# Optimization experiments

Measured on AMD Instinct MI355X. Metric: run time of the kernel, lower is better.

## Reference

```python
import jax, jax.numpy as jnp
import numpy as np

D_MODEL = 2048
D_FFN = 8192
RANK = 16
MOD_SCALE = 0.1
EPS = 1e-6


def setup_inputs() -> dict:
    key = jax.random.key(0)
    ks = jax.random.split(key, 8)
    B, S = 2, 2048
    init_scale = 0.01
    return {
        'hidden_states': jax.random.normal(ks[0], (B, S, D_MODEL), jnp.float32),
        'attn_output': jax.random.normal(ks[1], (B, S, D_MODEL), jnp.float32),
        'A': jax.random.normal(ks[2], (D_MODEL, RANK), jnp.float32) * (init_scale / np.sqrt(D_MODEL)),
        'Bmat': jax.random.normal(ks[3], (RANK, D_FFN), jnp.float32) * (init_scale / np.sqrt(RANK)),
        'W_in': jax.random.normal(ks[4], (D_FFN, D_MODEL), jnp.float32) * 0.02,  # gate_proj.weight
        'W_up': jax.random.normal(ks[5], (D_FFN, D_MODEL), jnp.float32) * 0.02,  # up_proj.weight
        'W_down': jax.random.normal(ks[6], (D_MODEL, D_FFN), jnp.float32) * 0.02,  # down_proj.weight
        'gamma': jnp.ones((D_MODEL,), jnp.float32),  # post_attention_layernorm (RMSNorm) weight
    }


def _rmsnorm(x, gamma):
    var = jnp.mean(x * x, axis=-1, keepdims=True)
    return x * jax.lax.rsqrt(var + EPS) * gamma


def reference(hidden_states, attn_output, A, Bmat, W_in, W_up, W_down, gamma):
    residual = hidden_states
    # Neuro-plastic modulation: [B,S,r]
    modulation = MOD_SCALE * jnp.tanh(jnp.einsum('bsd,dr->bsr', attn_output, A))
    # NPT applies post-attn norm to the residual (not residual+attn)
    h = _rmsnorm(residual, gamma)  # [B,S,d_model]
    # Fused per-token weight delta: delta_w^T @ h == B^T ((A^T h) * mod)
    hA = jnp.einsum('bsd,dr->bsr', h, A)  # [B,S,r]
    delta_out = jnp.einsum('bsr,rf->bsf', hA * modulation, Bmat)  # [B,S,d_ffn]
    gate = jax.nn.silu(jnp.einsum('bsd,fd->bsf', h, W_in) + delta_out)
    up = jnp.einsum('bsd,fd->bsf', h, W_up)
    out = jnp.einsum('bsf,df->bsd', gate * up, W_down)
    return residual + out
```

## Files before the change

kernel.cpp:

```cpp
#include <hip/hip_runtime.h>
#include <cstdint>
#include <cstddef>

#define D_MODEL 2048
#define D_FFN   8192
#define RANK    16
#define EPS     1e-6f
#define MOD_SCALE 0.1f

typedef float    f32x4 __attribute__((ext_vector_type(4)));
typedef _Float16 half8 __attribute__((ext_vector_type(8)));

__device__ __forceinline__ void async_load16(const void* g, void* l) {
  __builtin_amdgcn_global_load_lds(
      (const __attribute__((address_space(1))) uint32_t*)g,
      (__attribute__((address_space(3))) uint32_t*)l,
      16, 0, 0);
}

__device__ __forceinline__ void stage_tile(const _Float16* __restrict__ gbase,
                                           size_t stride, _Float16* lds, int tid) {
  #pragma unroll
  for (int j = 0; j < 4; ++j) {
    int idx = j * 256 + tid;
    int row = idx >> 3;
    int c   = (idx & 7) ^ (row & 7);
    async_load16(gbase + (size_t)row * stride + c * 8, &lds[idx * 8]);
  }
}

__device__ __forceinline__ half8 frag_read(const _Float16* lds, int r, int c) {
  return *(const half8*)&lds[r * 64 + ((c ^ (r & 7)) * 8)];
}

__global__ __launch_bounds__(256) void convert3_f32_f16(
    const float* __restrict__ s0, const float* __restrict__ s1,
    const float* __restrict__ s2,
    _Float16* __restrict__ d0, _Float16* __restrict__ d1,
    _Float16* __restrict__ d2)
{
  const int w = blockIdx.x >> 13;
  const float*   s = (w == 0) ? s0 : (w == 1) ? s1 : s2;
  _Float16*      d = (w == 0) ? d0 : (w == 1) ? d1 : d2;
  size_t i = ((size_t)(blockIdx.x & 8191) * 256 + threadIdx.x) * 8;
  f32x4 a = *(const f32x4*)(s + i);
  f32x4 b = *(const f32x4*)(s + i + 4);
  half8 h;
  #pragma unroll
  for (int j = 0; j < 4; ++j) { h[j] = (_Float16)a[j]; h[4+j] = (_Float16)b[j]; }
  *(half8*)(d + i) = h;
}

__global__ __launch_bounds__(256) void convert_f32_f16(
    const float* __restrict__ s, _Float16* __restrict__ d)
{
  size_t i = ((size_t)blockIdx.x * 256 + threadIdx.x) * 8;
  f32x4 a = *(const f32x4*)(s + i);
  f32x4 b = *(const f32x4*)(s + i + 4);
  half8 h;
  #pragma unroll
  for (int j = 0; j < 4; ++j) { h[j] = (_Float16)a[j]; h[4+j] = (_Float16)b[j]; }
  *(half8*)(d + i) = h;
}

__global__ __launch_bounds__(256) void prep_kernel(
    const float* __restrict__ hs, const float* __restrict__ attn,
    const float* __restrict__ Amat, const float* __restrict__ gamma,
    _Float16* __restrict__ h16, float* __restrict__ cmat)
{
  const int token = blockIdx.x;
  const int tid   = threadIdx.x;
  const int lane  = tid & 63;
  const int wv    = tid >> 6;
  const size_t tb = (size_t)token * D_MODEL;
  const int base  = tid * 8;

  f32x4 x0 = *(const f32x4*)(hs + tb + base);
  f32x4 x1 = *(const f32x4*)(hs + tb + base + 4);
  f32x4 a0 = *(const f32x4*)(attn + tb + base);
  f32x4 a1 = *(const f32x4*)(attn + tb + base + 4);

  float ss = 0.f;
  #pragma unroll
  for (int j = 0; j < 4; ++j) ss += x0[j]*x0[j] + x1[j]*x1[j];
  #pragma unroll
  for (int off = 32; off > 0; off >>= 1) ss += __shfl_xor(ss, off, 64);

  __shared__ float red[4];
  __shared__ float redp[4][RANK];
  __shared__ float redh[4][RANK];
  if (lane == 0) red[wv] = ss;
  __syncthreads();
  const float tot = red[0] + red[1] + red[2] + red[3];
  const float rms = rsqrtf(tot * (1.0f / D_MODEL) + EPS);

  f32x4 g0 = *(const f32x4*)(gamma + base);
  f32x4 g1 = *(const f32x4*)(gamma + base + 4);
  float hv[8], av[8];
  #pragma unroll
  for (int j = 0; j < 4; ++j) {
    hv[j]   = x0[j] * rms * g0[j];
    hv[4+j] = x1[j] * rms * g1[j];
    av[j]   = a0[j];
    av[4+j] = a1[j];
  }
  half8 hh;
  #pragma unroll
  for (int j = 0; j < 8; ++j) hh[j] = (_Float16)hv[j];
  *(half8*)(h16 + tb + base) = hh;

  float pa[RANK], ph[RANK];
  #pragma unroll
  for (int r = 0; r < RANK; ++r) { pa[r] = 0.f; ph[r] = 0.f; }
  #pragma unroll
  for (int e = 0; e < 8; ++e) {
    const f32x4* Ar = (const f32x4*)(Amat + (size_t)(base + e) * RANK);
    #pragma unroll
    for (int q = 0; q < 4; ++q) {
      f32x4 ar = Ar[q];
      #pragma unroll
      for (int j = 0; j < 4; ++j) {
        pa[q*4+j] += av[e] * ar[j];
        ph[q*4+j] += hv[e] * ar[j];
      }
    }
  }
  #pragma unroll
  for (int r = 0; r < RANK; ++r) {
    #pragma unroll
    for (int off = 32; off > 0; off >>= 1) {
      pa[r] += __shfl_xor(pa[r], off, 64);
      ph[r] += __shfl_xor(ph[r], off, 64);
    }
  }
  if (lane == 0) {
    #pragma unroll
    for (int r = 0; r < RANK; ++r) { redp[wv][r] = pa[r]; redh[wv][r] = ph[r]; }
  }
  __syncthreads();
  if (tid < RANK) {
    float sp = redp[0][tid] + redp[1][tid] + redp[2][tid] + redp[3][tid];
    float sh = redh[0][tid] + redh[1][tid] + redh[2][tid] + redh[3][tid];
    cmat[(size_t)token * RANK + tid] = sh * (MOD_SCALE * tanhf(sp));
  }
}

__global__ __launch_bounds__(256, 2) void gemm_gateup(
    const _Float16* __restrict__ h16,
    const _Float16* __restrict__ Wg16, const _Float16* __restrict__ Wu16,
    const float* __restrict__ cmat, const float* __restrict__ Bmat,
    _Float16* __restrict__ tmat)
{
  __shared__ __align__(16) _Float16 sA [128*64];
  __shared__ __align__(16) _Float16 sB1[128*64];
  __shared__ __align__(16) _Float16 sB2[128*64];

  const int tid  = threadIdx.x;
  const int lane = tid & 63;
  const int wv   = tid >> 6;
  const int wm   = (wv >> 1) * 64;
  const int wn   = (wv & 1) * 64;
  const int lr   = lane & 15;
  const int quad = lane >> 4;
  const int gm0  = blockIdx.y * 128;
  const int gn0  = blockIdx.x * 128;

  f32x4 accG[4][4], accU[4][4];
  #pragma unroll
  for (int i = 0; i < 4; ++i)
    #pragma unroll
    for (int j = 0; j < 4; ++j) {
      f32x4 z = {0.f, 0.f, 0.f, 0.f};
      accG[i][j] = z; accU[i][j] = z;
    }

  for (int kt = 0; kt < D_MODEL / 64; ++kt) {
    __syncthreads();
    stage_tile(h16  + (size_t)gm0 * D_MODEL + kt * 64, D_MODEL, sA,  tid);
    stage_tile(Wg16 + (size_t)gn0 * D_MODEL + kt * 64, D_MODEL, sB1, tid);
    stage_tile(Wu16 + (size_t)gn0 * D_MODEL + kt * 64, D_MODEL, sB2, tid);
    __syncthreads();
    #pragma unroll
    for (int ks = 0; ks < 2; ++ks) {
      const int ck = ks * 4 + quad;
      half8 af[4], bg[4], bu[4];
      #pragma unroll
      for (int im = 0; im < 4; ++im)
        af[im] = frag_read(sA, wm + im * 16 + lr, ck);
      #pragma unroll
      for (int in = 0; in < 4; ++in) {
        bg[in] = frag_read(sB1, wn + in * 16 + lr, ck);
        bu[in] = frag_read(sB2, wn + in * 16 + lr, ck);
      }
      #pragma unroll
      for (int im = 0; im < 4; ++im)
        #pragma unroll
        for (int in = 0; in < 4; ++in) {
          accG[im][in] = __builtin_amdgcn_mfma_f32_16x16x32_f16(af[im], bg[in], accG[im][in], 0, 0, 0);
          accU[im][in] = __builtin_amdgcn_mfma_f32_16x16x32_f16(af[im], bu[in], accU[im][in], 0, 0, 0);
        }
    }
  }

  __syncthreads();
  #pragma unroll
  for (int i = 0; i < 16; ++i) {
    int idx = i * 256 + tid;
    int m = idx >> 5, kk = idx & 31;
    sA[idx]  = (kk < RANK) ? (_Float16)cmat[(size_t)(gm0 + m) * RANK + kk] : (_Float16)0.0f;
    sB1[idx] = (kk < RANK) ? (_Float16)Bmat[(size_t)kk * D_FFN + gn0 + m]  : (_Float16)0.0f;
  }
  __syncthreads();
  {
    const int ko = quad * 8;
    half8 af[4], bd[4];
    #pragma unroll
    for (int im = 0; im < 4; ++im)
      af[im] = *(const half8*)&sA[(wm + im * 16 + lr) * 32 + ko];
    #pragma unroll
    for (int in = 0; in < 4; ++in)
      bd[in] = *(const half8*)&sB1[(wn + in * 16 + lr) * 32 + ko];
    #pragma unroll
    for (int im = 0; im < 4; ++im)
      #pragma unroll
      for (int in = 0; in < 4; ++in)
        accG[im][in] = __builtin_amdgcn_mfma_f32_16x16x32_f16(af[im], bd[in], accG[im][in], 0, 0, 0);
  }

  #pragma unroll
  for (int im = 0; im < 4; ++im)
    #pragma unroll
    for (int in = 0; in < 4; ++in) {
      const int growb = gm0 + wm + im * 16 + quad * 4;
      const int gcol  = gn0 + wn + in * 16 + lr;
      #pragma unroll
      for (int r = 0; r < 4; ++r) {
        float g = accG[im][in][r];
        float u = accU[im][in][r];
        float s = g / (1.0f + __expf(-g));
        tmat[(size_t)(growb + r) * D_FFN + gcol] = (_Float16)(s * u);
      }
    }
}

__global__ __launch_bounds__(256, 3) void gemm_down(
    const _Float16* __restrict__ tmat, const _Float16* __restrict__ Wd16,
    const float* __restrict__ hs, float* __restrict__ out)
{
  __shared__ __align__(16) _Float16 sA[128*64];
  __shared__ __align__(16) _Float16 sB[128*64];

  const int tid  = threadIdx.x;
  const int lane = tid & 63;
  const int wv   = tid >> 6;
  const int wm   = (wv >> 1) * 64;
  const int wn   = (wv & 1) * 64;
  const int lr   = lane & 15;
  const int quad = lane >> 4;
  const int gm0  = blockIdx.y * 128;
  const int gn0  = blockIdx.x * 128;

  f32x4 acc[4][4];
  #pragma unroll
  for (int i = 0; i < 4; ++i)
    #pragma unroll
    for (int j = 0; j < 4; ++j) {
      f32x4 z = {0.f, 0.f, 0.f, 0.f};
      acc[i][j] = z;
    }

  for (int kt = 0; kt < D_FFN / 64; ++kt) {
    __syncthreads();
    stage_tile(tmat + (size_t)gm0 * D_FFN + kt * 64, D_FFN, sA, tid);
    stage_tile(Wd16 + (size_t)gn0 * D_FFN + kt * 64, D_FFN, sB, tid);
    __syncthreads();
    #pragma unroll
    for (int ks = 0; ks < 2; ++ks) {
      const int ck = ks * 4 + quad;
      half8 af[4], bf_[4];
      #pragma unroll
      for (int im = 0; im < 4; ++im)
        af[im] = frag_read(sA, wm + im * 16 + lr, ck);
      #pragma unroll
      for (int in = 0; in < 4; ++in)
        bf_[in] = frag_read(sB, wn + in * 16 + lr, ck);
      #pragma unroll
      for (int im = 0; im < 4; ++im)
        #pragma unroll
        for (int in = 0; in < 4; ++in)
          acc[im][in] = __builtin_amdgcn_mfma_f32_16x16x32_f16(af[im], bf_[in], acc[im][in], 0, 0, 0);
    }
  }

  #pragma unroll
  for (int im = 0; im < 4; ++im)
    #pragma unroll
    for (int in = 0; in < 4; ++in) {
      const int growb = gm0 + wm + im * 16 + quad * 4;
      const int gcol  = gn0 + wn + in * 16 + lr;
      #pragma unroll
      for (int r = 0; r < 4; ++r) {
        size_t o = (size_t)(growb + r) * D_MODEL + gcol;
        out[o] = hs[o] + acc[im][in][r];
      }
    }
}

extern "C" void kernel_launch(void* const* d_in, const int* in_sizes, int n_in,
                              void* d_out, int out_size, void* d_ws, size_t ws_size,
                              hipStream_t stream) {
  const float* hs    = (const float*)d_in[0];
  const float* attn  = (const float*)d_in[1];
  const float* Amat  = (const float*)d_in[2];
  const float* Bmat  = (const float*)d_in[3];
  const float* Wg    = (const float*)d_in[4];
  const float* Wu    = (const float*)d_in[5];
  const float* Wd    = (const float*)d_in[6];
  const float* gamma = (const float*)d_in[7];
  float* out = (float*)d_out;

  const int M = in_sizes[0] / D_MODEL;
  const size_t WD = (size_t)D_FFN * D_MODEL;

  char* ws = (char*)d_ws;
  _Float16* h16  = (_Float16*)ws;
  float*    cmat = (float*)(ws + (size_t)M * D_MODEL * 2);
  _Float16* tmat = (_Float16*)(ws + (size_t)M * D_MODEL * 2 + (size_t)M * RANK * 4);
  _Float16* wbuf = tmat + (size_t)M * D_FFN;
  _Float16* Wg16 = wbuf;
  _Float16* Wu16 = wbuf + WD;

  const size_t base_bytes = (size_t)M * D_MODEL * 2 + (size_t)M * RANK * 4
                          + (size_t)M * D_FFN * 2 + 2 * WD * 2;
  const bool sep_wd = (ws_size >= base_bytes + WD * 2);
  _Float16* Wd16 = sep_wd ? (wbuf + 2 * WD) : wbuf;

  const int convBlocks = (int)(WD / (256 * 8));

  prep_kernel<<<M, 256, 0, stream>>>(hs, attn, Amat, gamma, h16, cmat);
  if (sep_wd) {
    convert3_f32_f16<<<3 * convBlocks, 256, 0, stream>>>(Wg, Wu, Wd, Wg16, Wu16, Wd16);
    gemm_gateup<<<dim3(D_FFN / 128, M / 128), 256, 0, stream>>>(h16, Wg16, Wu16, cmat, Bmat, tmat);
  } else {
    convert_f32_f16<<<convBlocks, 256, 0, stream>>>(Wg, Wg16);
    convert_f32_f16<<<convBlocks, 256, 0, stream>>>(Wu, Wu16);
    gemm_gateup<<<dim3(D_FFN / 128, M / 128), 256, 0, stream>>>(h16, Wg16, Wu16, cmat, Bmat, tmat);
    convert_f32_f16<<<convBlocks, 256, 0, stream>>>(Wd, Wd16);
  }
  gemm_down<<<dim3(D_MODEL / 128, M / 128), 256, 0, stream>>>(tmat, Wd16, hs, out);
}
```

Before: 749.2 us.

## Rewrite both GEMMs with 256x128 tiles, multi-buffered async LDS pipeline and tile swizzle

Both FFN GEMMs now use 512-thread blocks computing 256x128 output tiles. Global-to-LDS async loads run through a double-buffered (gate/up) or triple-buffered (down) pipeline, with explicit vmcnt waits, raw barriers and s_setprio around the MFMA phases. A 1D grid with a block-index swizzle is added for L2 locality. This aims to hide load latency behind MFMA work and raise arithmetic intensity, at the cost of more LDS (128KB for gate/up, 144KB for down), heavier register use, and hand-tuned wait counts that could be fragile.

```diff
diff --git a/kernel.cpp b/kernel.cpp
--- a/kernel.cpp
+++ b/kernel.cpp
@@ -18,20 +18,21 @@
       16, 0, 0);
 }
 
-__device__ __forceinline__ void stage_tile(const _Float16* __restrict__ gbase,
-                                           size_t stride, _Float16* lds, int tid) {
-  #pragma unroll
-  for (int j = 0; j < 4; ++j) {
-    int idx = j * 256 + tid;
-    int row = idx >> 3;
-    int c   = (idx & 7) ^ (row & 7);
-    async_load16(gbase + (size_t)row * stride + c * 8, &lds[idx * 8]);
-  }
-}
-
-__device__ __forceinline__ half8 frag_read(const _Float16* lds, int r, int c) {
-  return *(const half8*)&lds[r * 64 + ((c ^ (r & 7)) * 8)];
-}
+__device__ __forceinline__ void stage_round(const _Float16* __restrict__ g,
+                                            size_t stride, _Float16* l, int tid) {
+  const int row = tid >> 3;
+  const int cs  = (tid & 7) ^ (row & 7);
+  async_load16(g + (size_t)row * stride + (size_t)cs * 8, l + tid * 8);
+}
+
+__device__ __forceinline__ half8 frag64(const _Float16* base, int row, int ck) {
+  return *(const half8*)&base[row * 64 + ((ck ^ (row & 7)) * 8)];
+}
+
+#define BAR()   __builtin_amdgcn_s_barrier()
+#define PRIO1() __builtin_amdgcn_s_setprio(1)
+#define PRIO0() __builtin_amdgcn_s_setprio(0)
+#define VMW(n)  asm volatile("s_waitcnt vmcnt(" #n ")" ::: "memory")
 
 __global__ __launch_bounds__(256) void convert3_f32_f16(
     const float* __restrict__ s0, const float* __restrict__ s1,
@@ -145,165 +146,288 @@
   }
 }
 
-__global__ __launch_bounds__(256, 2) void gemm_gateup(
+#define BGOFF 16384
+#define BUOFF 24576
+
+__global__ __launch_bounds__(512, 2) void gemm_gateup(
     const _Float16* __restrict__ h16,
     const _Float16* __restrict__ Wg16, const _Float16* __restrict__ Wu16,
     const float* __restrict__ cmat, const float* __restrict__ Bmat,
     _Float16* __restrict__ tmat)
 {
-  __shared__ __align__(16) _Float16 sA [128*64];
-  __shared__ __align__(16) _Float16 sB1[128*64];
-  __shared__ __align__(16) _Float16 sB2[128*64];
+  __shared__ __align__(16) _Float16 lds[2][32768];
 
   const int tid  = threadIdx.x;
   const int lane = tid & 63;
   const int wv   = tid >> 6;
-  const int wm   = (wv >> 1) * 64;
-  const int wn   = (wv & 1) * 64;
   const int lr   = lane & 15;
   const int quad = lane >> 4;
-  const int gm0  = blockIdx.y * 128;
-  const int gn0  = blockIdx.x * 128;
-
-  f32x4 accG[4][4], accU[4][4];
-  #pragma unroll
-  for (int i = 0; i < 4; ++i)
-    #pragma unroll
-    for (int j = 0; j < 4; ++j) {
+  const int qb   = (wv >> 2) * 2;
+  const int e    = wv & 3;
+  const int wm   = (wv >> 2) * 128;
+
+  const int lin = blockIdx.x;
+  const int swz = (lin & 7) * 128 + (lin >> 3);
+  const int gm0 = (swz & 15) * 256;
+  const int gn0 = (swz >> 4) * 128;
+
+  constexpr int NT = D_MODEL / 64;
+
+  f32x4 accG[8][2], accU[8][2];
+  #pragma unroll
+  for (int i = 0; i < 8; ++i)
+    #pragma unroll
+    for (int j = 0; j < 2; ++j) {
       f32x4 z = {0.f, 0.f, 0.f, 0.f};
       accG[i][j] = z; accU[i][j] = z;
     }
 
-  for (int kt = 0; kt < D_MODEL / 64; ++kt) {
-    __syncthreads();
-    stage_tile(h16  + (size_t)gm0 * D_MODEL + kt * 64, D_MODEL, sA,  tid);
-    stage_tile(Wg16 + (size_t)gn0 * D_MODEL + kt * 64, D_MODEL, sB1, tid);
-    stage_tile(Wu16 + (size_t)gn0 * D_MODEL + kt * 64, D_MODEL, sB2, tid);
-    __syncthreads();
-    #pragma unroll
-    for (int ks = 0; ks < 2; ++ks) {
-      const int ck = ks * 4 + quad;
-      half8 af[4], bg[4], bu[4];
-      #pragma unroll
-      for (int im = 0; im < 4; ++im)
-        af[im] = frag_read(sA, wm + im * 16 + lr, ck);
-      #pragma unroll
-      for (int in = 0; in < 4; ++in) {
-        bg[in] = frag_read(sB1, wn + in * 16 + lr, ck);
-        bu[in] = frag_read(sB2, wn + in * 16 + lr, ck);
+#define STA(b,q,t)  stage_round(h16  + (size_t)(gm0 + (q)*64) * D_MODEL + (size_t)(t)*64, D_MODEL, &lds[b][(q)*4096], tid)
+#define STBG(b,p,t) stage_round(Wg16 + (size_t)(gn0 + (p)*64) * D_MODEL + (size_t)(t)*64, D_MODEL, &lds[b][BGOFF + (p)*4096], tid)
+#define STBU(b,p,t) stage_round(Wu16 + (size_t)(gn0 + (p)*64) * D_MODEL + (size_t)(t)*64, D_MODEL, &lds[b][BUOFF + (p)*4096], tid)
+
+  STA(0,0,0);  STA(0,2,0);
+  STBG(0,0,0); STBG(0,1,0);
+  STBU(0,0,0); STBU(0,1,0);
+  STA(0,1,0);  STA(0,3,0);
+  STA(1,0,1);  STA(1,2,1);
+  STBG(1,0,1); STBG(1,1,1);
+  VMW(8); BAR();
+
+  half8 af[4][2], bg[2][2], bu[2][2];
+
+  for (int t = 0; t < NT; ++t) {
+    const int cur = t & 1, nxt = cur ^ 1;
+    const _Float16* A   = &lds[cur][0];
+    const _Float16* Bgp = &lds[cur][BGOFF + e * 2048];
+    const _Float16* Bup = &lds[cur][BUOFF + e * 2048];
+    const bool s1 = (t + 1 < NT);
+    const bool s2 = (t + 2 < NT);
+    const bool deep = (t + 3 < NT);
+
+    #pragma unroll
+    for (int im = 0; im < 4; ++im)
+      #pragma unroll
+      for (int kk = 0; kk < 2; ++kk)
+        af[im][kk] = frag64(A + (qb + 0) * 4096, im*16 + lr, kk*4 + quad);
+    #pragma unroll
+    for (int inn = 0; inn < 2; ++inn)
+      #pragma unroll
+      for (int kk = 0; kk < 2; ++kk)
+        bg[inn][kk] = frag64(Bgp, inn*16 + lr, kk*4 + quad);
+    if (s1) { STBU(nxt, 0, t+1); STBU(nxt, 1, t+1); }
+    BAR();
+    PRIO1();
+    #pragma unroll
+    for (int im = 0; im < 4; ++im)
+      #pragma unroll
+      for (int inn = 0; inn < 2; ++inn)
+        #pragma unroll
+        for (int kk = 0; kk < 2; ++kk)
+          accG[im][inn] = __builtin_amdgcn_mfma_f32_16x16x32_f16(af[im][kk], bg[inn][kk], accG[im][inn], 0, 0, 0);
+    PRIO0();
+    if (deep) { VMW(8); } else { VMW(0); }
+    BAR();
+
+    #pragma unroll
+    for (int inn = 0; inn < 2; ++inn)
+      #pragma unroll
+      for (int kk = 0; kk < 2; ++kk)
+        bu[inn][kk] = frag64(Bup, inn*16 + lr, kk*4 + quad);
+    if (s1) { STA(nxt, 1, t+1); STA(nxt, 3, t+1); }
+    BAR();
+    PRIO1();
+    #pragma unroll
+    for (int im = 0; im < 4; ++im)
+      #pragma unroll
+      for (int inn = 0; inn < 2; ++inn)
+        #pragma unroll
+        for (int kk = 0; kk < 2; ++kk)
+          accU[im][inn] = __builtin_amdgcn_mfma_f32_16x16x32_f16(af[im][kk], bu[inn][kk], accU[im][inn], 0, 0, 0);
+    PRIO0();
+    if (deep) { VMW(8); } else { VMW(0); }
+    BAR();
+
+    #pragma unroll
+    for (int im = 0; im < 4; ++im)
+      #pragma unroll
+      for (int kk = 0; kk < 2; ++kk)
+        af[im][kk] = frag64(A + (qb + 1) * 4096, im*16 + lr, kk*4 + quad);
+    if (s2) { STA(cur, 0, t+2); STA(cur, 2, t+2); }
+    BAR();
+    PRIO1();
+    #pragma unroll
+    for (int im = 0; im < 4; ++im)
+      #pragma unroll
+      for (int inn = 0; inn < 2; ++inn)
+        #pragma unroll
+        for (int kk = 0; kk < 2; ++kk)
+          accG[4+im][inn] = __builtin_amdgcn_mfma_f32_16x16x32_f16(af[im][kk], bg[inn][kk], accG[4+im][inn], 0, 0, 0);
+    PRIO0();
+    BAR();
+
+    if (s2) { STBG(cur, 0, t+2); STBG(cur, 1, t+2); }
+    BAR();
+    PRIO1();
+    #pragma unroll
+    for (int im = 0; im < 4; ++im)
+      #pragma unroll
+      for (int inn = 0; inn < 2; ++inn)
+        #pragma unroll
+        for (int kk = 0; kk < 2; ++kk)
+          accU[4+im][inn] = __builtin_amdgcn_mfma_f32_16x16x32_f16(af[im][kk], bu[inn][kk], accU[4+im][inn], 0, 0, 0);
+    PRIO0();
+    if (deep) { VMW(8); } else { VMW(0); }
+    BAR();
+  }
+
+  __syncthreads();
+  _Float16* l0 = &lds[0][0];
+  for (int i = tid; i < 8192; i += 512) {
+    int m = i >> 5, k = i & 31;
+    l0[i] = (k < RANK) ? (_Float16)cmat[(size_t)(gm0 + m) * RANK + k] : (_Float16)0.f;
+  }
+  for (int i = tid; i < 4096; i += 512) {
+    int f = i >> 5, k = i & 31;
+    l0[8192 + i] = (k < RANK) ? (_Float16)Bmat[(size_t)k * D_FFN + gn0 + f] : (_Float16)0.f;
+  }
+  __syncthreads();
+  #pragma unroll
+  for (int ai = 0; ai < 8; ++ai) {
+    half8 cf = *(const half8*)&l0[(wm + ai*16 + lr) * 32 + quad * 8];
+    #pragma unroll
+    for (int inn = 0; inn < 2; ++inn) {
+      half8 bd = *(const half8*)&l0[8192 + (e*32 + inn*16 + lr) * 32 + quad * 8];
+      accG[ai][inn] = __builtin_amdgcn_mfma_f32_16x16x32_f16(cf, bd, accG[ai][inn], 0, 0, 0);
+    }
+  }
+
+  #pragma unroll
+  for (int ai = 0; ai < 8; ++ai)
+    #pragma unroll
+    for (int inn = 0; inn < 2; ++inn) {
+      const int grow = gm0 + wm + ai*16 + quad*4;
+      const int gcol = gn0 + e*32 + inn*16 + lr;
+      #pragma unroll
+      for (int r = 0; r < 4; ++r) {
+        float g = accG[ai][inn][r];
+        float u = accU[ai][inn][r];
+        float s = g / (1.0f + __expf(-g));
+        tmat[(size_t)(grow + r) * D_FFN + gcol] = (_Float16)(s * u);
       }
-      #pragma unroll
-      for (int im = 0; im < 4; ++im)
-        #pragma unroll
-        for (int in = 0; in < 4; ++in) {
-          accG[im][in] = __builtin_amdgcn_mfma_f32_16x16x32_f16(af[im], bg[in], accG[im][in], 0, 0, 0);
-          accU[im][in] = __builtin_amdgcn_mfma_f32_16x16x32_f16(af[im], bu[in], accU[im][in], 0, 0, 0);
-        }
-    }
-  }
-
-  __syncthreads();
-  #pragma unroll
-  for (int i = 0; i < 16; ++i) {
-    int idx = i * 256 + tid;
-    int m = idx >> 5, kk = idx & 31;
-    sA[idx]  = (kk < RANK) ? (_Float16)cmat[(size_t)(gm0 + m) * RANK + kk] : (_Float16)0.0f;
-    sB1[idx] = (kk < RANK) ? (_Float16)Bmat[(size_t)kk * D_FFN + gn0 + m]  : (_Float16)0.0f;
-  }
-  __syncthreads();
-  {
-    const int ko = quad * 8;
-    half8 af[4], bd[4];
-    #pragma unroll
-    for (int im = 0; im < 4; ++im)
-      af[im] = *(const half8*)&sA[(wm + im * 16 + lr) * 32 + ko];
-    #pragma unroll
-    for (int in = 0; in < 4; ++in)
-      bd[in] = *(const half8*)&sB1[(wn + in * 16 + lr) * 32 + ko];
-    #pragma unroll
-    for (int im = 0; im < 4; ++im)
-      #pragma unroll
-      for (int in = 0; in < 4; ++in)
-        accG[im][in] = __builtin_amdgcn_mfma_f32_16x16x32_f16(af[im], bd[in], accG[im][in], 0, 0, 0);
-  }
-
-  #pragma unroll
-  for (int im = 0; im < 4; ++im)
-    #pragma unroll
-    for (int in = 0; in < 4; ++in) {
-      const int growb = gm0 + wm + im * 16 + quad * 4;
-      const int gcol  = gn0 + wn + in * 16 + lr;
-      #pragma unroll
-      for (int r = 0; r < 4; ++r) {
-        float g = accG[im][in][r];
-        float u = accU[im][in][r];
-        float s = g / (1.0f + __expf(-g));
-        tmat[(size_t)(growb + r) * D_FFN + gcol] = (_Float16)(s * u);
-      }
-    }
-}
-
-__global__ __launch_bounds__(256, 3) void gemm_down(
+    }
+#undef STA
+#undef STBG
+#undef STBU
+}
+
+__global__ __launch_bounds__(512, 2) void gemm_down(
     const _Float16* __restrict__ tmat, const _Float16* __restrict__ Wd16,
     const float* __restrict__ hs, float* __restrict__ out)
 {
-  __shared__ __align__(16) _Float16 sA[128*64];
-  __shared__ __align__(16) _Float16 sB[128*64];
+  __shared__ __align__(16) _Float16 lds[3][24576];
 
   const int tid  = threadIdx.x;
   const int lane = tid & 63;
   const int wv   = tid >> 6;
-  const int wm   = (wv >> 1) * 64;
-  const int wn   = (wv & 1) * 64;
   const int lr   = lane & 15;
   const int quad = lane >> 4;
-  const int gm0  = blockIdx.y * 128;
-  const int gn0  = blockIdx.x * 128;
-
-  f32x4 acc[4][4];
-  #pragma unroll
-  for (int i = 0; i < 4; ++i)
-    #pragma unroll
-    for (int j = 0; j < 4; ++j) {
+  const int qb   = (wv >> 2) * 2;
+  const int e    = wv & 3;
+  const int wm   = (wv >> 2) * 128;
+
+  const int lin = blockIdx.x;
+  const int swz = (lin & 7) * 32 + (lin >> 3);
+  const int gm0 = (swz & 15) * 256;
+  const int gn0 = (swz >> 4) * 128;
+
+  constexpr int NT = D_FFN / 64;
+
+  f32x4 acc[8][2];
+  #pragma unroll
+  for (int i = 0; i < 8; ++i)
+    #pragma unroll
+    for (int j = 0; j < 2; ++j) {
       f32x4 z = {0.f, 0.f, 0.f, 0.f};
       acc[i][j] = z;
     }
 
-  for (int kt = 0; kt < D_FFN / 64; ++kt) {
-    __syncthreads();
-    stage_tile(tmat + (size_t)gm0 * D_FFN + kt * 64, D_FFN, sA, tid);
-    stage_tile(Wd16 + (size_t)gn0 * D_FFN + kt * 64, D_FFN, sB, tid);
-    __syncthreads();
-    #pragma unroll
-    for (int ks = 0; ks < 2; ++ks) {
-      const int ck = ks * 4 + quad;
-      half8 af[4], bf_[4];
-      #pragma unroll
-      for (int im = 0; im < 4; ++im)
-        af[im] = frag_read(sA, wm + im * 16 + lr, ck);
-      #pragma unroll
-      for (int in = 0; in < 4; ++in)
-        bf_[in] = frag_read(sB, wn + in * 16 + lr, ck);
-      #pragma unroll
-      for (int im = 0; im < 4; ++im)
-        #pragma unroll
-        for (int in = 0; in < 4; ++in)
-          acc[im][in] = __builtin_amdgcn_mfma_f32_16x16x32_f16(af[im], bf_[in], acc[im][in], 0, 0, 0);
-    }
-  }
-
-  #pragma unroll
-  for (int im = 0; im < 4; ++im)
-    #pragma unroll
-    for (int in = 0; in < 4; ++in) {
-      const int growb = gm0 + wm + im * 16 + quad * 4;
-      const int gcol  = gn0 + wn + in * 16 + lr;
+#define DSTA(b,q,t) stage_round(tmat + (size_t)(gm0 + (q)*64) * D_FFN + (size_t)(t)*64, D_FFN, &lds[b][(q)*4096], tid)
+#define DSTB(b,p,t) stage_round(Wd16 + (size_t)(gn0 + (p)*64) * D_FFN + (size_t)(t)*64, D_FFN, &lds[b][16384 + (p)*4096], tid)
+
+  DSTA(0,0,0); DSTA(0,1,0); DSTA(0,2,0); DSTA(0,3,0); DSTB(0,0,0); DSTB(0,1,0);
+  DSTA(1,0,1); DSTA(1,1,1); DSTA(1,2,1); DSTA(1,3,1); DSTB(1,0,1); DSTB(1,1,1);
+  VMW(6); BAR();
+
+  half8 af[4][2], bf[2][2];
+  int cur = 0;
+
+  for (int t = 0; t < NT; ++t) {
+    const _Float16* A = &lds[cur][0];
+    const _Float16* B = &lds[cur][16384 + e * 2048];
+    int nx2 = cur + 2; if (nx2 >= 3) nx2 -= 3;
+    const bool s2 = (t + 2 < NT);
+    const bool deep = (t + 3 < NT);
+
+    #pragma unroll
+    for (int im = 0; im < 4; ++im)
+      #pragma unroll
+      for (int kk = 0; kk < 2; ++kk)
+        af[im][kk] = frag64(A + (qb + 0) * 4096, im*16 + lr, kk*4 + quad);
+    #pragma unroll
+    for (int inn = 0; inn < 2; ++inn)
+      #pragma unroll
+      for (int kk = 0; kk < 2; ++kk)
+        bf[inn][kk] = frag64(B, inn*16 + lr, kk*4 + quad);
+    if (s2) { DSTA(nx2, 0, t+2); DSTA(nx2, 2, t+2); DSTB(nx2, 0, t+2); }
+    BAR();
+    PRIO1();
+    #pragma unroll
+    for (int im = 0; im < 4; ++im)
+      #pragma unroll
+      for (int inn = 0; inn < 2; ++inn)
+        #pragma unroll
+        for (int kk = 0; kk < 2; ++kk)
+          acc[im][inn] = __builtin_amdgcn_mfma_f32_16x16x32_f16(af[im][kk], bf[inn][kk], acc[im][inn], 0, 0, 0);
+    PRIO0();
+    BAR();
+
+    #pragma unroll
+    for (int im = 0; im < 4; ++im)
+      #pragma unroll
+      for (int kk = 0; kk < 2; ++kk)
+        af[im][kk] = frag64(A + (qb + 1) * 4096, im*16 + lr, kk*4 + quad);
+    if (s2) { DSTA(nx2, 1, t+2); DSTA(nx2, 3, t+2); DSTB(nx2, 1, t+2); }
+    BAR();
+    PRIO1();
+    #pragma unroll
+    for (int im = 0; im < 4; ++im)
+      #pragma unroll
+      for (int inn = 0; inn < 2; ++inn)
+        #pragma unroll
+        for (int kk = 0; kk < 2; ++kk)
+          acc[4+im][inn] = __builtin_amdgcn_mfma_f32_16x16x32_f16(af[im][kk], bf[inn][kk], acc[4+im][inn], 0, 0, 0);
+    PRIO0();
+    if (deep) { VMW(6); } else { VMW(0); }
+    BAR();
+
+    cur += 1; if (cur >= 3) cur -= 3;
+  }
+
+  #pragma unroll
+  for (int ai = 0; ai < 8; ++ai)
+    #pragma unroll
+    for (int inn = 0; inn < 2; ++inn) {
+      const int grow = gm0 + wm + ai*16 + quad*4;
+      const int gcol = gn0 + e*32 + inn*16 + lr;
       #pragma unroll
       for (int r = 0; r < 4; ++r) {
-        size_t o = (size_t)(growb + r) * D_MODEL + gcol;
-        out[o] = hs[o] + acc[im][in][r];
+        size_t o = (size_t)(grow + r) * D_MODEL + gcol;
+        out[o] = hs[o] + acc[ai][inn][r];
       }
     }
+#undef DSTA
+#undef DSTB
 }
 
 extern "C" void kernel_launch(void* const* d_in, const int* in_sizes, int n_in,
@@ -340,12 +464,12 @@
   prep_kernel<<<M, 256, 0, stream>>>(hs, attn, Amat, gamma, h16, cmat);
   if (sep_wd) {
     convert3_f32_f16<<<3 * convBlocks, 256, 0, stream>>>(Wg, Wu, Wd, Wg16, Wu16, Wd16);
-    gemm_gateup<<<dim3(D_FFN / 128, M / 128), 256, 0, stream>>>(h16, Wg16, Wu16, cmat, Bmat, tmat);
+    gemm_gateup<<<dim3((D_FFN / 128) * (M / 256)), 512, 0, stream>>>(h16, Wg16, Wu16, cmat, Bmat, tmat);
   } else {
     convert_f32_f16<<<convBlocks, 256, 0, stream>>>(Wg, Wg16);
     convert_f32_f16<<<convBlocks, 256, 0, stream>>>(Wu, Wu16);
-    gemm_gateup<<<dim3(D_FFN / 128, M / 128), 256, 0, stream>>>(h16, Wg16, Wu16, cmat, Bmat, tmat);
+    gemm_gateup<<<dim3((D_FFN / 128) * (M / 256)), 512, 0, stream>>>(h16, Wg16, Wu16, cmat, Bmat, tmat);
     convert_f32_f16<<<convBlocks, 256, 0, stream>>>(Wd, Wd16);
   }
-  gemm_down<<<dim3(D_MODEL / 128, M / 128), 256, 0, stream>>>(tmat, Wd16, hs, out);
-}
+  gemm_down<<<dim3((D_MODEL / 128) * (M / 256)), 512, 0, stream>>>(tmat, Wd16, hs, out);
+}
```

Result: no change. 745.1 us (-0.6%).
